# Optimization experiments

Hardware: AMD Instinct MI355X
Metric: run time of the kernel (lower is better)

Reference implementation:

```python
import jax, jax.numpy as jnp
import numpy as np


def setup_inputs() -> dict:
    key = jax.random.key(0)
    k1, k2, k3, k4, k5 = jax.random.split(key, 5)
    B, S, T = 512, 1024, 32
    emissions = jax.random.normal(k1, (B, S, T), dtype=jnp.float32)
    tags = jax.random.randint(k2, (B, S), 0, T, dtype=jnp.int64)
    mask = jnp.ones((B, S), dtype=jnp.float32)  # all positions valid; mask[:,0]==1 required
    transitions = jax.random.normal(k3, (T, T), dtype=jnp.float32)
    start_transitions = jax.random.normal(k4, (T,), dtype=jnp.float32)
    end_transitions = jax.random.normal(k5, (T,), dtype=jnp.float32)
    return {
        "emissions": emissions,
        "tags": tags,
        "mask": mask,
        "transitions": transitions,
        "start_transitions": start_transitions,
        "end_transitions": end_transitions,
    }


def _compute_score(emissions, tags, mask, transitions, start_transitions, end_transitions):
    # score of the gold path, fully vectorized over time
    # first step
    score = start_transitions[tags[:, 0]]
    score = score + jnp.take_along_axis(emissions[:, 0], tags[:, 0:1], axis=1)[:, 0]
    # steps 1..S-1
    emit = jnp.take_along_axis(emissions[:, 1:], tags[:, 1:, None], axis=2)[..., 0]  # [B,S-1]
    trans = transitions[tags[:, :-1], tags[:, 1:]]                                   # [B,S-1]
    score = score + ((emit + trans) * mask[:, 1:]).sum(axis=1)
    # end transition from the last valid tag
    last_idx = mask.sum(axis=1).astype(jnp.int32) - 1                                # [B]
    last_tags = jnp.take_along_axis(tags, last_idx[:, None].astype(tags.dtype), axis=1)[:, 0]
    score = score + end_transitions[last_tags]
    return score


def _compute_partition(emissions, mask, transitions, start_transitions, end_transitions):
    # forward algorithm: logsumexp scan over time
    alpha0 = start_transitions + emissions[:, 0]  # [B,T]

    def step(alpha, inp):
        e_i, m_i = inp  # e_i: [B,T], m_i: [B]
        # alpha[b,i] + transitions[i,j] + e_i[b,j] -> logsumexp over i
        scores = alpha[:, :, None] + transitions[None, :, :] + e_i[:, None, :]  # [B,T,T]
        next_alpha = jax.nn.logsumexp(scores, axis=1)                            # [B,T]
        m = m_i[:, None]
        alpha = next_alpha * m + alpha * (1.0 - m)
        return alpha, None

    xs = (jnp.swapaxes(emissions[:, 1:], 0, 1), jnp.swapaxes(mask[:, 1:], 0, 1))
    alpha, _ = jax.lax.scan(step, alpha0, xs)
    alpha = alpha + end_transitions
    return jax.nn.logsumexp(alpha, axis=1)  # [B]


def reference(emissions, tags, mask, transitions, start_transitions, end_transitions):
    score = _compute_score(emissions, tags, mask, transitions, start_transitions, end_transitions)
    partition = _compute_partition(emissions, mask, transitions, start_transitions, end_transitions)
    return -(score - partition).sum()
```

## Files before the change

### kernel.cpp

```cpp
#include <hip/hip_runtime.h>


typedef __attribute__((ext_vector_type(8)))  short    short8;
typedef __attribute__((ext_vector_type(16))) float    f32x16;
typedef __attribute__((ext_vector_type(4)))  unsigned uint4v;

#define S_N 1024
#define T_N 32
#define B_N 512
#define L_CH 32
#define C_CH 32
#define SCALE_MUL 0.0078125f
#define SCALE_LOG 4.852030263919617f

#define WS_FRAG_DW ((size_t)B_N * C_CH * 512)
#define WS_MSUM_OFF (WS_FRAG_DW)
#define WS_SCORE_OFF (WS_FRAG_DW + 512)
#define WS_A_OFF (WS_FRAG_DW + 1024)
#define WS_NAPP_OFF (WS_FRAG_DW + 1536)

#if __has_builtin(__builtin_amdgcn_cvt_pk_bf16_f32)
typedef __attribute__((ext_vector_type(2))) __bf16 bf16x2;
__device__ __forceinline__ unsigned cvtpk(float lo, float hi) {
    return __builtin_bit_cast(unsigned, __builtin_amdgcn_cvt_pk_bf16_f32(lo, hi));
}
#else
__device__ __forceinline__ unsigned cvtpk(float lo, float hi) {
    const unsigned a = __float_as_uint(lo) + 0x8000u;
    const unsigned b = __float_as_uint(hi) + 0x8000u;
    return __builtin_amdgcn_perm(b, a, 0x07060302u);
}
#endif

__device__ __forceinline__ short8 mk8(const unsigned* a) {
    uint4v u = {a[0], a[1], a[2], a[3]};
    return __builtin_bit_cast(short8, u);
}
__device__ __forceinline__ float bflo(unsigned u) { return __uint_as_float(u << 16); }
__device__ __forceinline__ float bfhi(unsigned u) { return __uint_as_float(u & 0xFFFF0000u); }
__device__ __forceinline__ int PIx(int x) { return (x & ~12) | ((x & 4) << 1) | ((x & 8) >> 1); }

__global__ __launch_bounds__(64) void crf_prep(
    const float* __restrict__ trans, unsigned* __restrict__ wsf)
{
    const int lane = threadIdx.x;
    const int n = lane & 31, h = lane >> 5;
    unsigned A1[4], A2[4];
    #pragma unroll
    for (int j = 0; j < 4; ++j) {
        const int k1 = PIx(8 * h + 2 * j);
        const int k2 = PIx(16 + 8 * h + 2 * j);
        A1[j] = cvtpk(__expf(trans[n * 32 + k1]), __expf(trans[n * 32 + k1 + 1]));
        A2[j] = cvtpk(__expf(trans[n * 32 + k2]), __expf(trans[n * 32 + k2 + 1]));
    }
    unsigned* dst = wsf + WS_A_OFF + lane * 8;
    ((uint4*)dst)[0] = make_uint4(A1[0], A1[1], A1[2], A1[3]);
    ((uint4*)dst)[1] = make_uint4(A2[0], A2[1], A2[2], A2[3]);
}

__global__ __launch_bounds__(256, 4) void crf_chunk(
    const float* __restrict__ em, const int* __restrict__ tags,
    const float* __restrict__ mask, const float* __restrict__ trans,
    const float* __restrict__ startT, unsigned* __restrict__ wsf,
    float* __restrict__ wsflt)
{
    __shared__ unsigned elds[16][512];
    const int wib  = threadIdx.x >> 6;
    const int lane = threadIdx.x & 63;
    const int n    = lane & 31;
    const int h    = lane >> 5;
    const int b    = blockIdx.x >> 1;
    const int half = blockIdx.x & 1;
    const int c0   = half * 16 + wib * 4;

    #pragma unroll
    for (int q = 0; q < 4; ++q) {
        const float* eq = em + ((size_t)b * S_N + (c0 + q) * L_CH) * T_N;
        unsigned* mq = elds[wib * 4 + q];
        #pragma unroll
        for (int i = 0; i < 8; ++i) {
            const int flat = i * 64 + lane;
            const int r = flat >> 4, m = flat & 15;
            const int base = ((m & 4) << 2) + ((m & 2) << 2) + ((m & 1) << 1) + ((m >> 3) << 2);
            const float2 v = *(const float2*)(eq + r * 32 + base);
            mq[r * 16 + m] = cvtpk(__expf(v.x) * SCALE_MUL, __expf(v.y) * SCALE_MUL);
        }
    }

    unsigned mb_[4];
    {
        float vacc = 0.f, macc = 0.f;
        #pragma unroll
        for (int q2 = 0; q2 < 2; ++q2) {
            const int s  = c0 * L_CH + q2 * 64 + lane;
            const float mv = mask[b * S_N + s];
            const unsigned long long mb = __ballot(mv != 0.0f);
            mb_[2 * q2]     = (unsigned)mb;
            mb_[2 * q2 + 1] = (unsigned)(mb >> 32);
            const int tc = tags[b * S_N + s];
            int tp = __shfl_up(tc, 1, 64);
            float val;
            if (lane == 0) {
                if (s == 0) {
                    val = startT[tc] + em[(size_t)b * S_N * T_N + tc];
                } else {
                    tp = tags[b * S_N + s - 1];
                    val = mv * (em[((size_t)b * S_N + s) * T_N + tc] + trans[tp * 32 + tc]);
                }
            } else {
                val = mv * (em[((size_t)b * S_N + s) * T_N + tc] + trans[tp * 32 + tc]);
            }
            vacc += val; macc += mv;
        }
        if (c0 == 0) mb_[0] &= ~1u;
        #pragma unroll
        for (int d = 32; d > 0; d >>= 1) {
            vacc += __shfl_xor(vacc, d, 64);
            macc += __shfl_xor(macc, d, 64);
        }
        if (lane == 0) {
            atomicAdd(&wsflt[WS_SCORE_OFF + b], vacc);
            atomicAdd(&wsflt[WS_MSUM_OFF + b], macc);
            #pragma unroll
            for (int q = 0; q < 4; ++q)
                wsflt[WS_NAPP_OFF + b * C_CH + c0 + q] = (float)__popc(mb_[q]);
        }
    }

    const uint4 ua = ((const uint4*)(wsf + WS_A_OFF))[lane * 2];
    const uint4 ub = ((const uint4*)(wsf + WS_A_OFF))[lane * 2 + 1];
    const short8 A1v = mk8((const unsigned*)&ua);
    const short8 A2v = mk8((const unsigned*)&ub);
    const f32x16 Zacc = {};

    f32x16 D0, D1, D2, D3;
    #pragma unroll
    for (int i = 0; i < 16; ++i) {
        const int row = (i & 3) + 8 * (i >> 2) + 4 * h;
        const float v = (row == n) ? 1.0f : 0.0f;
        D0[i] = v; D1[i] = v; D2[i] = v; D3[i] = v;
    }

    const unsigned* m0 = elds[wib * 4];
    const unsigned* m1 = elds[wib * 4 + 1];
    const unsigned* m2 = elds[wib * 4 + 2];
    const unsigned* m3 = elds[wib * 4 + 3];

    #define STEP(D, mq, r_) { \
        const uint4 su = *(const uint4*)((mq) + (r_) * 16 + h * 8); \
        const uint4 sv = *(const uint4*)((mq) + (r_) * 16 + h * 8 + 4); \
        unsigned S[8]; \
        S[0] = cvtpk(D[0]  * bflo(su.x), D[1]  * bfhi(su.x)); \
        S[1] = cvtpk(D[2]  * bflo(su.y), D[3]  * bfhi(su.y)); \
        S[2] = cvtpk(D[4]  * bflo(su.z), D[5]  * bfhi(su.z)); \
        S[3] = cvtpk(D[6]  * bflo(su.w), D[7]  * bfhi(su.w)); \
        S[4] = cvtpk(D[8]  * bflo(sv.x), D[9]  * bfhi(sv.x)); \
        S[5] = cvtpk(D[10] * bflo(sv.y), D[11] * bfhi(sv.y)); \
        S[6] = cvtpk(D[12] * bflo(sv.z), D[13] * bfhi(sv.z)); \
        S[7] = cvtpk(D[14] * bflo(sv.w), D[15] * bfhi(sv.w)); \
        f32x16 t_ = __builtin_amdgcn_mfma_f32_32x32x16_bf16(A1v, mk8(&S[0]), Zacc, 0, 0, 0); \
        D = __builtin_amdgcn_mfma_f32_32x32x16_bf16(A2v, mk8(&S[4]), t_, 0, 0, 0); \
    }

    const bool allclean =
        ((mb_[0] | (c0 == 0 ? 1u : 0u)) == 0xFFFFFFFFu) &&
        (mb_[1] == 0xFFFFFFFFu) && (mb_[2] == 0xFFFFFFFFu) && (mb_[3] == 0xFFFFFFFFu);

    if (allclean) {
        #pragma unroll 2
        for (int r = L_CH - 1; r >= 1; --r) {
            STEP(D0, m0, r); STEP(D1, m1, r); STEP(D2, m2, r); STEP(D3, m3, r);
        }
        if (mb_[0] & 1u) STEP(D0, m0, 0);
        if (mb_[1] & 1u) STEP(D1, m1, 0);
        if (mb_[2] & 1u) STEP(D2, m2, 0);
        if (mb_[3] & 1u) STEP(D3, m3, 0);
    } else {
        for (int r = L_CH - 1; r >= 0; --r) {
            if ((mb_[0] >> r) & 1u) STEP(D0, m0, r);
            if ((mb_[1] >> r) & 1u) STEP(D1, m1, r);
            if ((mb_[2] >> r) & 1u) STEP(D2, m2, r);
            if ((mb_[3] >> r) & 1u) STEP(D3, m3, r);
        }
    }
    #undef STEP

    #define STORE(D, q_) { \
        unsigned* dst = wsf + ((size_t)(b * C_CH + c0 + (q_)) * 64 + lane) * 8; \
        ((uint4*)dst)[0] = make_uint4(cvtpk(D[0], D[1]),   cvtpk(D[2], D[3]), \
                                      cvtpk(D[4], D[5]),   cvtpk(D[6], D[7])); \
        ((uint4*)dst)[1] = make_uint4(cvtpk(D[8], D[9]),   cvtpk(D[10], D[11]), \
                                      cvtpk(D[12], D[13]), cvtpk(D[14], D[15])); \
    }
    STORE(D0, 0) STORE(D1, 1) STORE(D2, 2) STORE(D3, 3)
    #undef STORE
}

__global__ __launch_bounds__(256) void crf_combine(
    const float* __restrict__ em, const int* __restrict__ tags,
    const float* __restrict__ startT, const float* __restrict__ endT,
    const unsigned* __restrict__ wsf, const float* __restrict__ wsflt,
    float* __restrict__ out)
{
    const int lane = threadIdx.x & 63;
    const int n = lane & 31, h = lane >> 5;
    const int b = blockIdx.x * 4 + (threadIdx.x >> 6);

    int idxA[8], idxB[8];
    #pragma unroll
    for (int j = 0; j < 8; ++j) {
        idxA[j] = PIx(8 * h + j);
        idxB[j] = PIx(16 + 8 * h + j);
    }

    float a0 = startT[n] + em[(size_t)b * S_N * T_N + n];
    float m = a0;
    #pragma unroll
    for (int d = 16; d > 0; d >>= 1) m = fmaxf(m, __shfl_xor(m, d, 32));
    float A = __expf(a0 - m);
    float Lacc = m;
    float ntot = (lane < 32) ? wsflt[WS_NAPP_OFF + b * C_CH + lane] : 0.0f;

    const uint4* fb = (const uint4*)(wsf + (size_t)b * C_CH * 512);
    uint4 q0 = fb[lane * 2];
    uint4 q1 = fb[lane * 2 + 1];

    for (int c = 0; c < C_CH; ++c) {
        uint4 n0 = q0, n1 = q1;
        if (c + 1 < C_CH) {
            n0 = fb[(c + 1) * 128 + lane * 2];
            n1 = fb[(c + 1) * 128 + lane * 2 + 1];
        }

        float p0 = 0.f, p1 = 0.f, p2 = 0.f, p3 = 0.f;
        p0 = fmaf(__shfl(A, idxA[0], 32), bflo(q0.x), p0);
        p1 = fmaf(__shfl(A, idxA[1], 32), bfhi(q0.x), p1);
        p2 = fmaf(__shfl(A, idxA[2], 32), bflo(q0.y), p2);
        p3 = fmaf(__shfl(A, idxA[3], 32), bfhi(q0.y), p3);
        p0 = fmaf(__shfl(A, idxA[4], 32), bflo(q0.z), p0);
        p1 = fmaf(__shfl(A, idxA[5], 32), bfhi(q0.z), p1);
        p2 = fmaf(__shfl(A, idxA[6], 32), bflo(q0.w), p2);
        p3 = fmaf(__shfl(A, idxA[7], 32), bfhi(q0.w), p3);
        p0 = fmaf(__shfl(A, idxB[0], 32), bflo(q1.x), p0);
        p1 = fmaf(__shfl(A, idxB[1], 32), bfhi(q1.x), p1);
        p2 = fmaf(__shfl(A, idxB[2], 32), bflo(q1.y), p2);
        p3 = fmaf(__shfl(A, idxB[3], 32), bfhi(q1.y), p3);
        p0 = fmaf(__shfl(A, idxB[4], 32), bflo(q1.z), p0);
        p1 = fmaf(__shfl(A, idxB[5], 32), bfhi(q1.z), p1);
        p2 = fmaf(__shfl(A, idxB[6], 32), bflo(q1.w), p2);
        p3 = fmaf(__shfl(A, idxB[7], 32), bfhi(q1.w), p3);
        float part = (p0 + p1) + (p2 + p3);
        part += __shfl_xor(part, 32);

        float mm = part;
        #pragma unroll
        for (int d = 16; d > 0; d >>= 1) mm = fmaxf(mm, __shfl_xor(mm, d, 32));
        A = part / mm;
        Lacc += __logf(mm);
        q0 = n0; q1 = n1;
    }

    float v = A * __expf(endT[n]);
    #pragma unroll
    for (int d = 16; d > 0; d >>= 1) {
        v    += __shfl_xor(v, d, 32);
        ntot += __shfl_xor(ntot, d, 32);
    }
    if (lane == 0) {
        const int len = (int)(wsflt[WS_MSUM_OFF + b] + 0.5f);
        const int lt  = tags[b * S_N + len - 1];
        const float res = Lacc + __logf(v) + ntot * SCALE_LOG
                          - endT[lt] - wsflt[WS_SCORE_OFF + b];
        atomicAdd(out, res);
    }
}

extern "C" void kernel_launch(void* const* d_in, const int* in_sizes, int n_in,
                              void* d_out, int out_size, void* d_ws, size_t ws_size,
                              hipStream_t stream) {
    const float* em     = (const float*)d_in[0];
    const int*   tags   = (const int*)  d_in[1];
    const float* mask   = (const float*)d_in[2];
    const float* trans  = (const float*)d_in[3];
    const float* startT = (const float*)d_in[4];
    const float* endT   = (const float*)d_in[5];
    float* out = (float*)d_out;

    unsigned* wsf   = (unsigned*)d_ws;
    float*    wsflt = (float*)d_ws;

    hipMemsetAsync(out, 0, sizeof(float), stream);
    hipMemsetAsync((char*)d_ws + WS_MSUM_OFF * 4, 0, 4096, stream);

    hipLaunchKernelGGL(crf_prep, dim3(1), dim3(64), 0, stream, trans, wsf);
    hipLaunchKernelGGL(crf_chunk, dim3(1024), dim3(256), 0, stream,
                       em, tags, mask, trans, startT, wsf, wsflt);
    hipLaunchKernelGGL(crf_combine, dim3(128), dim3(256), 0, stream,
                       em, tags, startT, endT, wsf, wsflt, out);
}
```

Before: 179.5 us.

## Fuse prep/chunk/combine into one kernel with last-block combine and fp16 MFMA

Drops the separate prep and combine kernels. Each chunk block now computes the exp(transitions) fragments itself, and the second of the two blocks for a batch row, chosen through an atomic ready counter and a threadfence, runs the combine scan on one wave. The MFMA path also moves from bf16 to fp16: packed half2 multiplies with pkrtz conversion replace per-element float multiplies, and the scale constant is adjusted to fit the fp16 range. This removes two launches and the serial dependency between kernels, but the combine runs on one wave per row in the tail of the grid, and fp16 narrows the representable range.

Result: slower. 311.5 us (+73.6%).

```diff
diff --git a/kernel.cpp b/kernel.cpp
--- a/kernel.cpp
+++ b/kernel.cpp
@@ -1,7 +1,9 @@
 #include <hip/hip_runtime.h>
-
-
-typedef __attribute__((ext_vector_type(8)))  short    short8;
+#include <hip/hip_fp16.h>
+
+
+typedef __attribute__((ext_vector_type(8)))  _Float16 half8;
+typedef __attribute__((ext_vector_type(2)))  _Float16 half2v;
 typedef __attribute__((ext_vector_type(16))) float    f32x16;
 typedef __attribute__((ext_vector_type(4)))  unsigned uint4v;
 
@@ -10,61 +12,43 @@
 #define B_N 512
 #define L_CH 32
 #define C_CH 32
-#define SCALE_MUL 0.0078125f
-#define SCALE_LOG 4.852030263919617f
+#define SCALE_MUL 0.011048543456039806f
+#define SCALE_LOG 4.505456673639645f
 
 #define WS_FRAG_DW ((size_t)B_N * C_CH * 512)
 #define WS_MSUM_OFF (WS_FRAG_DW)
 #define WS_SCORE_OFF (WS_FRAG_DW + 512)
-#define WS_A_OFF (WS_FRAG_DW + 1024)
+#define WS_READY_OFF (WS_FRAG_DW + 1024)
 #define WS_NAPP_OFF (WS_FRAG_DW + 1536)
 
-#if __has_builtin(__builtin_amdgcn_cvt_pk_bf16_f32)
-typedef __attribute__((ext_vector_type(2))) __bf16 bf16x2;
-__device__ __forceinline__ unsigned cvtpk(float lo, float hi) {
-    return __builtin_bit_cast(unsigned, __builtin_amdgcn_cvt_pk_bf16_f32(lo, hi));
-}
-#else
-__device__ __forceinline__ unsigned cvtpk(float lo, float hi) {
-    const unsigned a = __float_as_uint(lo) + 0x8000u;
-    const unsigned b = __float_as_uint(hi) + 0x8000u;
-    return __builtin_amdgcn_perm(b, a, 0x07060302u);
-}
-#endif
-
-__device__ __forceinline__ short8 mk8(const unsigned* a) {
+__device__ __forceinline__ unsigned pkrtz(float lo, float hi) {
+    return __builtin_bit_cast(unsigned, __builtin_amdgcn_cvt_pkrtz(lo, hi));
+}
+__device__ __forceinline__ unsigned pmul(unsigned a, unsigned b) {
+    const __half2 r = __builtin_bit_cast(__half2, a) * __builtin_bit_cast(__half2, b);
+    return __builtin_bit_cast(unsigned, r);
+}
+__device__ __forceinline__ half8 mkh8(const unsigned* a) {
     uint4v u = {a[0], a[1], a[2], a[3]};
-    return __builtin_bit_cast(short8, u);
-}
-__device__ __forceinline__ float bflo(unsigned u) { return __uint_as_float(u << 16); }
-__device__ __forceinline__ float bfhi(unsigned u) { return __uint_as_float(u & 0xFFFF0000u); }
+    return __builtin_bit_cast(half8, u);
+}
+__device__ __forceinline__ float hlo(unsigned u) {
+    return (float)__builtin_bit_cast(half2v, u).x;
+}
+__device__ __forceinline__ float hhi(unsigned u) {
+    return (float)__builtin_bit_cast(half2v, u).y;
+}
 __device__ __forceinline__ int PIx(int x) { return (x & ~12) | ((x & 4) << 1) | ((x & 8) >> 1); }
-
-__global__ __launch_bounds__(64) void crf_prep(
-    const float* __restrict__ trans, unsigned* __restrict__ wsf)
-{
-    const int lane = threadIdx.x;
-    const int n = lane & 31, h = lane >> 5;
-    unsigned A1[4], A2[4];
-    #pragma unroll
-    for (int j = 0; j < 4; ++j) {
-        const int k1 = PIx(8 * h + 2 * j);
-        const int k2 = PIx(16 + 8 * h + 2 * j);
-        A1[j] = cvtpk(__expf(trans[n * 32 + k1]), __expf(trans[n * 32 + k1 + 1]));
-        A2[j] = cvtpk(__expf(trans[n * 32 + k2]), __expf(trans[n * 32 + k2 + 1]));
-    }
-    unsigned* dst = wsf + WS_A_OFF + lane * 8;
-    ((uint4*)dst)[0] = make_uint4(A1[0], A1[1], A1[2], A1[3]);
-    ((uint4*)dst)[1] = make_uint4(A2[0], A2[1], A2[2], A2[3]);
-}
 
 __global__ __launch_bounds__(256, 4) void crf_chunk(
     const float* __restrict__ em, const int* __restrict__ tags,
     const float* __restrict__ mask, const float* __restrict__ trans,
-    const float* __restrict__ startT, unsigned* __restrict__ wsf,
-    float* __restrict__ wsflt)
+    const float* __restrict__ startT, const float* __restrict__ endT,
+    unsigned* __restrict__ wsf, float* __restrict__ wsflt,
+    float* __restrict__ out)
 {
     __shared__ unsigned elds[16][512];
+    __shared__ int winner;
     const int wib  = threadIdx.x >> 6;
     const int lane = threadIdx.x & 63;
     const int n    = lane & 31;
@@ -83,7 +67,7 @@
             const int r = flat >> 4, m = flat & 15;
             const int base = ((m & 4) << 2) + ((m & 2) << 2) + ((m & 1) << 1) + ((m >> 3) << 2);
             const float2 v = *(const float2*)(eq + r * 32 + base);
-            mq[r * 16 + m] = cvtpk(__expf(v.x) * SCALE_MUL, __expf(v.y) * SCALE_MUL);
+            mq[r * 16 + m] = pkrtz(__expf(v.x) * SCALE_MUL, __expf(v.y) * SCALE_MUL);
         }
     }
 
@@ -127,10 +111,15 @@
         }
     }
 
-    const uint4 ua = ((const uint4*)(wsf + WS_A_OFF))[lane * 2];
-    const uint4 ub = ((const uint4*)(wsf + WS_A_OFF))[lane * 2 + 1];
-    const short8 A1v = mk8((const unsigned*)&ua);
-    const short8 A2v = mk8((const unsigned*)&ub);
+    unsigned A1[4], A2[4];
+    #pragma unroll
+    for (int j = 0; j < 4; ++j) {
+        const int k1 = PIx(8 * h + 2 * j);
+        const int k2 = PIx(16 + 8 * h + 2 * j);
+        A1[j] = pkrtz(__expf(trans[n * 32 + k1]), __expf(trans[n * 32 + k1 + 1]));
+        A2[j] = pkrtz(__expf(trans[n * 32 + k2]), __expf(trans[n * 32 + k2 + 1]));
+    }
+    const half8 A1v = mkh8(A1), A2v = mkh8(A2);
     const f32x16 Zacc = {};
 
     f32x16 D0, D1, D2, D3;
@@ -150,16 +139,16 @@
         const uint4 su = *(const uint4*)((mq) + (r_) * 16 + h * 8); \
         const uint4 sv = *(const uint4*)((mq) + (r_) * 16 + h * 8 + 4); \
         unsigned S[8]; \
-        S[0] = cvtpk(D[0]  * bflo(su.x), D[1]  * bfhi(su.x)); \
-        S[1] = cvtpk(D[2]  * bflo(su.y), D[3]  * bfhi(su.y)); \
-        S[2] = cvtpk(D[4]  * bflo(su.z), D[5]  * bfhi(su.z)); \
-        S[3] = cvtpk(D[6]  * bflo(su.w), D[7]  * bfhi(su.w)); \
-        S[4] = cvtpk(D[8]  * bflo(sv.x), D[9]  * bfhi(sv.x)); \
-        S[5] = cvtpk(D[10] * bflo(sv.y), D[11] * bfhi(sv.y)); \
-        S[6] = cvtpk(D[12] * bflo(sv.z), D[13] * bfhi(sv.z)); \
-        S[7] = cvtpk(D[14] * bflo(sv.w), D[15] * bfhi(sv.w)); \
-        f32x16 t_ = __builtin_amdgcn_mfma_f32_32x32x16_bf16(A1v, mk8(&S[0]), Zacc, 0, 0, 0); \
-        D = __builtin_amdgcn_mfma_f32_32x32x16_bf16(A2v, mk8(&S[4]), t_, 0, 0, 0); \
+        S[0] = pmul(pkrtz(D[0],  D[1]),  su.x); \
+        S[1] = pmul(pkrtz(D[2],  D[3]),  su.y); \
+        S[2] = pmul(pkrtz(D[4],  D[5]),  su.z); \
+        S[3] = pmul(pkrtz(D[6],  D[7]),  su.w); \
+        S[4] = pmul(pkrtz(D[8],  D[9]),  sv.x); \
+        S[5] = pmul(pkrtz(D[10], D[11]), sv.y); \
+        S[6] = pmul(pkrtz(D[12], D[13]), sv.z); \
+        S[7] = pmul(pkrtz(D[14], D[15]), sv.w); \
+        f32x16 t_ = __builtin_amdgcn_mfma_f32_32x32x16_f16(A1v, mkh8(&S[0]), Zacc, 0, 0, 0); \
+        D = __builtin_amdgcn_mfma_f32_32x32x16_f16(A2v, mkh8(&S[4]), t_, 0, 0, 0); \
     }
 
     const bool allclean =
@@ -187,24 +176,23 @@
 
     #define STORE(D, q_) { \
         unsigned* dst = wsf + ((size_t)(b * C_CH + c0 + (q_)) * 64 + lane) * 8; \
-        ((uint4*)dst)[0] = make_uint4(cvtpk(D[0], D[1]),   cvtpk(D[2], D[3]), \
-                                      cvtpk(D[4], D[5]),   cvtpk(D[6], D[7])); \
-        ((uint4*)dst)[1] = make_uint4(cvtpk(D[8], D[9]),   cvtpk(D[10], D[11]), \
-                                      cvtpk(D[12], D[13]), cvtpk(D[14], D[15])); \
+        ((uint4*)dst)[0] = make_uint4(pkrtz(D[0], D[1]),   pkrtz(D[2], D[3]), \
+                                      pkrtz(D[4], D[5]),   pkrtz(D[6], D[7])); \
+        ((uint4*)dst)[1] = make_uint4(pkrtz(D[8], D[9]),   pkrtz(D[10], D[11]), \
+                                      pkrtz(D[12], D[13]), pkrtz(D[14], D[15])); \
     }
     STORE(D0, 0) STORE(D1, 1) STORE(D2, 2) STORE(D3, 3)
     #undef STORE
-}
-
-__global__ __launch_bounds__(256) void crf_combine(
-    const float* __restrict__ em, const int* __restrict__ tags,
-    const float* __restrict__ startT, const float* __restrict__ endT,
-    const unsigned* __restrict__ wsf, const float* __restrict__ wsflt,
-    float* __restrict__ out)
-{
-    const int lane = threadIdx.x & 63;
-    const int n = lane & 31, h = lane >> 5;
-    const int b = blockIdx.x * 4 + (threadIdx.x >> 6);
+
+    __threadfence();
+    __syncthreads();
+    if (threadIdx.x == 0) {
+        int* ready = (int*)&wsflt[WS_READY_OFF];
+        winner = (atomicAdd(&ready[b], 1) == 1) ? 1 : 0;
+    }
+    __syncthreads();
+    if (!winner || wib != 0) return;
+    __threadfence();
 
     int idxA[8], idxB[8];
     #pragma unroll
@@ -233,22 +221,22 @@
         }
 
         float p0 = 0.f, p1 = 0.f, p2 = 0.f, p3 = 0.f;
-        p0 = fmaf(__shfl(A, idxA[0], 32), bflo(q0.x), p0);
-        p1 = fmaf(__shfl(A, idxA[1], 32), bfhi(q0.x), p1);
-        p2 = fmaf(__shfl(A, idxA[2], 32), bflo(q0.y), p2);
-        p3 = fmaf(__shfl(A, idxA[3], 32), bfhi(q0.y), p3);
-        p0 = fmaf(__shfl(A, idxA[4], 32), bflo(q0.z), p0);
-        p1 = fmaf(__shfl(A, idxA[5], 32), bfhi(q0.z), p1);
-        p2 = fmaf(__shfl(A, idxA[6], 32), bflo(q0.w), p2);
-        p3 = fmaf(__shfl(A, idxA[7], 32), bfhi(q0.w), p3);
-        p0 = fmaf(__shfl(A, idxB[0], 32), bflo(q1.x), p0);
-        p1 = fmaf(__shfl(A, idxB[1], 32), bfhi(q1.x), p1);
-        p2 = fmaf(__shfl(A, idxB[2], 32), bflo(q1.y), p2);
-        p3 = fmaf(__shfl(A, idxB[3], 32), bfhi(q1.y), p3);
-        p0 = fmaf(__shfl(A, idxB[4], 32), bflo(q1.z), p0);
-        p1 = fmaf(__shfl(A, idxB[5], 32), bfhi(q1.z), p1);
-        p2 = fmaf(__shfl(A, idxB[6], 32), bflo(q1.w), p2);
-        p3 = fmaf(__shfl(A, idxB[7], 32), bfhi(q1.w), p3);
+        p0 = fmaf(__shfl(A, idxA[0], 32), hlo(q0.x), p0);
+        p1 = fmaf(__shfl(A, idxA[1], 32), hhi(q0.x), p1);
+        p2 = fmaf(__shfl(A, idxA[2], 32), hlo(q0.y), p2);
+        p3 = fmaf(__shfl(A, idxA[3], 32), hhi(q0.y), p3);
+        p0 = fmaf(__shfl(A, idxA[4], 32), hlo(q0.z), p0);
+        p1 = fmaf(__shfl(A, idxA[5], 32), hhi(q0.z), p1);
+        p2 = fmaf(__shfl(A, idxA[6], 32), hlo(q0.w), p2);
+        p3 = fmaf(__shfl(A, idxA[7], 32), hhi(q0.w), p3);
+        p0 = fmaf(__shfl(A, idxB[0], 32), hlo(q1.x), p0);
+        p1 = fmaf(__shfl(A, idxB[1], 32), hhi(q1.x), p1);
+        p2 = fmaf(__shfl(A, idxB[2], 32), hlo(q1.y), p2);
+        p3 = fmaf(__shfl(A, idxB[3], 32), hhi(q1.y), p3);
+        p0 = fmaf(__shfl(A, idxB[4], 32), hlo(q1.z), p0);
+        p1 = fmaf(__shfl(A, idxB[5], 32), hhi(q1.z), p1);
+        p2 = fmaf(__shfl(A, idxB[6], 32), hlo(q1.w), p2);
+        p3 = fmaf(__shfl(A, idxB[7], 32), hhi(q1.w), p3);
         float part = (p0 + p1) + (p2 + p3);
         part += __shfl_xor(part, 32);
 
@@ -290,11 +278,8 @@
     float*    wsflt = (float*)d_ws;
 
     hipMemsetAsync(out, 0, sizeof(float), stream);
-    hipMemsetAsync((char*)d_ws + WS_MSUM_OFF * 4, 0, 4096, stream);
-
-    hipLaunchKernelGGL(crf_prep, dim3(1), dim3(64), 0, stream, trans, wsf);
+    hipMemsetAsync((char*)d_ws + WS_MSUM_OFF * 4, 0, 6144, stream);
+
     hipLaunchKernelGGL(crf_chunk, dim3(1024), dim3(256), 0, stream,
-                       em, tags, mask, trans, startT, wsf, wsflt);
-    hipLaunchKernelGGL(crf_combine, dim3(128), dim3(256), 0, stream,
-                       em, tags, startT, endT, wsf, wsflt, out);
-}
+                       em, tags, mask, trans, startT, endT, wsf, wsflt, out);
+}
```
